# Kernel optimization log

Hardware: AMD Instinct MI355X
Metric: run time of the kernel (lower is better)

Reference implementation:

```python
import jax, jax.numpy as jnp
import numpy as np

B, N, E, P, PH, H = 4, 512, 768, 64, 32, 8
D = E // H  # 96
FFN = 3072

def _ln(x, g, b, eps=1e-5):
    mu = jnp.mean(x, axis=-1, keepdims=True)
    var = jnp.mean((x - mu) ** 2, axis=-1, keepdims=True)
    return (x - mu) * jax.lax.rsqrt(var + eps) * g + b

def setup_inputs() -> dict:
    key = jax.random.key(0)
    ks = iter(jax.random.split(key, 80))
    def f(*s):
        return jax.random.normal(next(ks), s, jnp.float32) * 0.02
    ones = lambda *s: jnp.ones(s, jnp.float32)
    zeros = lambda *s: jnp.zeros(s, jnp.float32)
    return {
        'x': jax.random.normal(next(ks), (B, N, E), jnp.float32),
        'pair': jax.random.normal(next(ks), (B, N, N, P), jnp.float32) * 0.5,
        'attn_mask': zeros(B, 1, N, N),
        'op_mask': ones(B, N, 1),
        'op_norm': ones(1) / N,
        'nlist': jax.random.randint(next(ks), (B, N, 64), 0, N),
        'wq': f(E, E), 'wk': f(E, E), 'wv': f(E, E),
        'wg': f(E, E), 'bg': zeros(E),
        'wo': f(E, E), 'bo': zeros(E),
        'ln_pair_g': ones(P), 'ln_pair_b': zeros(P),
        'wb': f(H, P), 'bb': zeros(H),
        'ln_attn_g': ones(E), 'ln_attn_b': zeros(E),
        'ln_ffn_g': ones(E), 'ln_ffn_b': zeros(E),
        'w_ffn1': f(FFN, E), 'b_ffn1': zeros(FFN),
        'w_ffn2': f(E, FFN), 'b_ffn2': zeros(E),
        'ln_opm_g': ones(E), 'ln_opm_b': zeros(E),
        'w_opm_in': f(2 * PH, E), 'b_opm_in': zeros(2 * PH),
        'w_opm_out': f(P, PH * PH), 'b_opm_out': zeros(P),
        'ln_tm_g': ones(P), 'ln_tm_b': zeros(P),
        'w_tm_abp': f(2 * PH, P), 'b_tm_abp': zeros(2 * PH),
        'w_tm_abg': f(2 * PH, P), 'b_tm_abg': zeros(2 * PH),
        'w_tm_g': f(P, P), 'b_tm_g': zeros(P),
        'w_tm_z': f(P, PH), 'b_tm_z': zeros(P),
        'ln_tmo_g': ones(PH), 'ln_tmo_b': zeros(PH),
        'ln_pffn_g': ones(P), 'ln_pffn_b': zeros(P),
        'w_pffn1': f(P, P), 'b_pffn1': zeros(P),
        'w_pffn2': f(P, P), 'b_pffn2': zeros(P),
    }

def _forward(x, pair, attn_mask, op_mask, op_norm, wq, wk, wv, wg, bg, wo, bo,
             ln_pair_g, ln_pair_b, wb, bb, ln_attn_g, ln_attn_b,
             ln_ffn_g, ln_ffn_b, w_ffn1, b_ffn1, w_ffn2, b_ffn2,
             ln_opm_g, ln_opm_b, w_opm_in, b_opm_in, w_opm_out, b_opm_out,
             ln_tm_g, ln_tm_b, w_tm_abp, b_tm_abp, w_tm_abg, b_tm_abg,
             w_tm_g, b_tm_g, w_tm_z, b_tm_z, ln_tmo_g, ln_tmo_b,
             ln_pffn_g, ln_pffn_b, w_pffn1, b_pffn1, w_pffn2, b_pffn2):
    Bx, Nx, _ = x.shape
    # --- gated pair-bias self-attention (pre-LN, eval mode: dropout = identity) ---
    h = _ln(x, ln_attn_g, ln_attn_b)
    pn = _ln(pair, ln_pair_g, ln_pair_b)               # AtomAttention pair LayerNorm
    bias = jnp.einsum('bijp,hp->bhij', pn, wb) + bb[None, :, None, None]
    q = (h @ wq.T).reshape(Bx, Nx, H, D).transpose(0, 2, 1, 3) * (D ** -0.5)
    k = (h @ wk.T).reshape(Bx, Nx, H, D).transpose(0, 2, 1, 3)
    v = (h @ wv.T).reshape(Bx, Nx, H, D).transpose(0, 2, 1, 3)
    attn = jax.nn.softmax(jnp.einsum('bhid,bhjd->bhij', q, k) + attn_mask + bias, axis=-1)
    o = jnp.einsum('bhij,bhjd->bhid', attn, v).transpose(0, 2, 1, 3).reshape(Bx, Nx, E)
    o = jax.nn.sigmoid(h @ wg.T + bg) * o              # sigmoid output gate
    x = x + (o @ wo.T + bo)
    # --- atom transition MLP ---
    h = _ln(x, ln_ffn_g, ln_ffn_b)
    x = x + (jax.nn.gelu(h @ w_ffn1.T + b_ffn1, approximate=False) @ w_ffn2.T + b_ffn2)
    # --- OuterProduct pair update (fused: avoids [B,N,N,PH*PH] intermediate) ---
    h = _ln(x, ln_opm_g, ln_opm_b)
    ab = (h @ w_opm_in.T + b_opm_in) * op_mask
    a_o, b_o = jnp.split(ab, 2, axis=-1)               # each [B,N,PH]
    z = jnp.einsum('bid,bje,pde->bijp', a_o, b_o, w_opm_out.reshape(P, PH, PH)) + b_opm_out
    pair = pair + z * op_norm
    # --- triangle multiplication ---
    zp = _ln(pair, ln_tm_g, ln_tm_b)
    gpr = zp @ w_tm_g.T + b_tm_g                       # gate (no sigmoid, matches source)
    ab = (zp @ w_tm_abp.T + b_tm_abp) * jax.nn.sigmoid(zp @ w_tm_abg.T + b_tm_abg)
    a_t, b_t = jnp.split(ab, 2, axis=-1)               # each [B,N,N,PH]
    t = jnp.einsum('bijh,bkjh->bhik', a_t, b_t) + jnp.einsum('bjih,bjkh->bhik', a_t, b_t)
    t = _ln(t.transpose(0, 2, 3, 1), ln_tmo_g, ln_tmo_b) @ w_tm_z.T + b_tm_z
    pair = pair + gpr * t
    # --- pair transition MLP ---
    zp = _ln(pair, ln_pffn_g, ln_pffn_b)
    pair = pair + (jax.nn.gelu(zp @ w_pffn1.T + b_pffn1, approximate=False) @ w_pffn2.T + b_pffn2)
    return x, pair

def reference(x, pair, attn_mask, op_mask, op_norm, nlist, wq, wk, wv, wg, bg, wo, bo,
              ln_pair_g, ln_pair_b, wb, bb, ln_attn_g, ln_attn_b,
              ln_ffn_g, ln_ffn_b, w_ffn1, b_ffn1, w_ffn2, b_ffn2,
              ln_opm_g, ln_opm_b, w_opm_in, b_opm_in, w_opm_out, b_opm_out,
              ln_tm_g, ln_tm_b, w_tm_abp, b_tm_abp, w_tm_abg, b_tm_abg,
              w_tm_g, b_tm_g, w_tm_z, b_tm_z, ln_tmo_g, ln_tmo_b,
              ln_pffn_g, ln_pffn_b, w_pffn1, b_pffn1, w_pffn2, b_pffn2):
    del nlist  # accepted by the torch module but unused in the math
    return _forward(x, pair, attn_mask, op_mask, op_norm, wq, wk, wv, wg, bg, wo, bo,
                    ln_pair_g, ln_pair_b, wb, bb, ln_attn_g, ln_attn_b,
                    ln_ffn_g, ln_ffn_b, w_ffn1, b_ffn1, w_ffn2, b_ffn2,
                    ln_opm_g, ln_opm_b, w_opm_in, b_opm_in, w_opm_out, b_opm_out,
                    ln_tm_g, ln_tm_b, w_tm_abp, b_tm_abp, w_tm_abg, b_tm_abg,
                    w_tm_g, b_tm_g, w_tm_z, b_tm_z, ln_tmo_g, ln_tmo_b,
                    ln_pffn_g, ln_pffn_b, w_pffn1, b_pffn1, w_pffn2, b_pffn2)
```

## Files before the change

kernel.cpp:

```cpp
#include <hip/hip_runtime.h>
#include <hip/hip_bf16.h>
#include <math.h>

#define Nn 512
#define Ee 768
#define Pp 64
#define PHh 32
#define Hh 8
#define Dd 96
#define NNe 262144
#define LNEPS 1e-5f

typedef __attribute__((ext_vector_type(8))) short bf8;
typedef __attribute__((ext_vector_type(4))) short bf4;
typedef __attribute__((ext_vector_type(4))) float f32x4;
#define MFMA(a,b,c) __builtin_amdgcn_mfma_f32_16x16x32_bf16(a,b,c,0,0,0)

__device__ __forceinline__ short f2bf(float f) {
  unsigned u = __builtin_bit_cast(unsigned, f);
  unsigned r = (u + 0x7fffu + ((u >> 16) & 1u)) >> 16;
  return (short)r;
}
__device__ __forceinline__ float bf2f(short s) {
  unsigned u = ((unsigned)(unsigned short)s) << 16;
// ... 117 lines not shown
      bf8 b0 = *(const bf8*)&Bs[(wc * 32 + llo) * 72 + ks * 32 + lhi * 8];
      bf8 b1 = *(const bf8*)&Bs[(wc * 32 + 16 + llo) * 72 + ks * 32 + lhi * 8];
      acc[0][0] = MFMA(a0, b0, acc[0][0]);
      acc[0][1] = MFMA(a0, b1, acc[0][1]);
      acc[1][0] = MFMA(a1, b0, acc[1][0]);
      acc[1][1] = MFMA(a1, b1, acc[1][1]);
    }
    __syncthreads();
  }
#pragma unroll
  for (int mi = 0; mi < 2; ++mi) {
    int gmb = m0 + wr * 32 + mi * 16 + lhi * 4;
#pragma unroll
    for (int ni = 0; ni < 2; ++ni) {
      int gn = n0 + wc * 32 + ni * 16 + llo;
      if (gn >= N) continue;
      float bv = bias ? bias[gn] : 0.f;
      float vr[4];
#pragma unroll
      for (int r = 0; r < 4; ++r) {
        float v = acc[mi][ni][r] + bv;
        if (resid) {
          float rv = resid[(long)(gmb + r) * ldr + gn];
          if (act == 2) v = sigmoidf_(rv) * acc[mi][ni][r];
          else v += rv;
        }
        if (act == 1) v = gelu_exact(v);
        vr[r] = v;
      }
      if (outF) {
#pragma unroll
        for (int r = 0; r < 4; ++r) outF[(long)(gmb + r) * ldf + gn] = vr[r];
      }
      if (outB) {
        if (vtrans) {
          bf4 pk;
#pragma unroll
          for (int r = 0; r < 4; ++r) pk[r] = f2bf(vr[r]);
          *(bf4*)(outB + ((long)((gmb >> 9) * 768 + gn) * 512 + (gmb & 511))) = pk;
        } else {
#pragma unroll
          for (int r = 0; r < 4; ++r) outB[(long)(gmb + r) * ldob + gn] = f2bf(vr[r]);
        }
      }
    }
  }
}

__global__ __launch_bounds__(256) void gemm_qkvg(
    const short* __restrict__ A, const short* __restrict__ W,
    short* __restrict__ q_bf, short* __restrict__ k_bf,
    short* __restrict__ vT_bf, float* __restrict__ gb,
    const float* __restrict__ bg) {
  __shared__ __align__(16) short As[64 * 72];
  __shared__ __align__(16) short Bs[64 * 72];
  int m0 = blockIdx.y * 64, n0 = blockIdx.x * 64;
  int sec = n0 / 768;
  int cbase = n0 - sec * 768;
  int tid = threadIdx.x;
  int wv = tid >> 6, lane = tid & 63;
  int wr = wv >> 1, wc = wv & 1;
  int lhi = lane >> 4, llo = lane & 15;
  int r4 = tid >> 2, c8 = (tid & 3) * 8;
  f32x4 acc[2][2] = {};
  for (int k0 = 0; k0 < 768; k0 += 64) {
    *(bf8*)&As[r4 * 72 + c8] = *(const bf8*)(A + (long)(m0 + r4) * 768 + k0 + c8);
    *(bf8*)&As[r4 * 72 + 32 + c8] =
        *(const bf8*)(A + (long)(m0 + r4) * 768 + k0 + 32 + c8);
    *(bf8*)&Bs[r4 * 72 + c8] = *(const bf8*)(W + (long)(n0 + r4) * 768 + k0 + c8);
    *(bf8*)&Bs[r4 * 72 + 32 + c8] =
        *(const bf8*)(W + (long)(n0 + r4) * 768 + k0 + 32 + c8);
    __syncthreads();
#pragma unroll
    for (int ks = 0; ks < 2; ++ks) {
      bf8 a0 = *(const bf8*)&As[(wr * 32 + llo) * 72 + ks * 32 + lhi * 8];
      bf8 a1 = *(const bf8*)&As[(wr * 32 + 16 + llo) * 72 + ks * 32 + lhi * 8];
      bf8 b0 = *(const bf8*)&Bs[(wc * 32 + llo) * 72 + ks * 32 + lhi * 8];
      bf8 b1 = *(const bf8*)&Bs[(wc * 32 + 16 + llo) * 72 + ks * 32 + lhi * 8];
      acc[0][0] = MFMA(a0, b0, acc[0][0]);
      acc[0][1] = MFMA(a0, b1, acc[0][1]);
      acc[1][0] = MFMA(a1, b0, acc[1][0]);
      acc[1][1] = MFMA(a1, b1, acc[1][1]);
    }
    __syncthreads();
  }
#pragma unroll
  for (int mi = 0; mi < 2; ++mi) {
    int gmb = m0 + wr * 32 + mi * 16 + lhi * 4;
#pragma unroll
    for (int ni = 0; ni < 2; ++ni) {
      int cn = cbase + wc * 32 + ni * 16 + llo;
      if (sec == 0) {
#pragma unroll
        for (int r = 0; r < 4; ++r) q_bf[(long)(gmb + r) * 768 + cn] = f2bf(acc[mi][ni][r]);
      } else if (sec == 1) {
#pragma unroll
        for (int r = 0; r < 4; ++r) k_bf[(long)(gmb + r) * 768 + cn] = f2bf(acc[mi][ni][r]);
      } else if (sec == 2) {
        bf4 pk;
#pragma unroll
        for (int r = 0; r < 4; ++r) pk[r] = f2bf(acc[mi][ni][r]);
        *(bf4*)(vT_bf + ((long)((gmb >> 9) * 768 + cn) * 512 + (gmb & 511))) = pk;
      } else {
        float bv = bg[cn];
#pragma unroll
        for (int r = 0; r < 4; ++r) gb[(long)(gmb + r) * 768 + cn] = acc[mi][ni][r] + bv;
      }
    }
  }
}

__global__ __launch_bounds__(256) void attn_fused(
    const short* __restrict__ q_bf, const short* __restrict__ k_bf,
    const short* __restrict__ bias_bf, const float* __restrict__ mask,
    short* __restrict__ out_bf) {
  int it = blockIdx.x, h = blockIdx.y, b = blockIdx.z;
  int tid = threadIdx.x;
  int wv = tid >> 6, lane = tid & 63;
  int lhi = lane >> 4, llo = lane & 15;
  int i0 = it * 16;
  long qoff = ((long)(b * 512 + i0)) * 768 + h * 96;
  bf8 qf[3];
#pragma unroll
  for (int ks = 0; ks < 3; ++ks)
    qf[ks] = *(const bf8*)(q_bf + qoff + (long)llo * 768 + ks * 32 + lhi * 8);
  long koff = ((long)b * 512) * 768 + h * 96;
  long bioff = (long)(b * 8 + h) * NNe + (long)i0 * 512;
  long moff = (long)b * NNe + (long)i0 * 512;
  float sv[8][4];
  int jb0 = wv * 128;
#pragma unroll
  for (int jf = 0; jf < 8; ++jf) {
    int jb = jb0 + jf * 16;
    f32x4 acc = {0.f, 0.f, 0.f, 0.f};
#pragma unroll
    for (int ks = 0; ks < 3; ++ks) {
      bf8 kf = *(const bf8*)(k_bf + koff + (long)(jb + llo) * 768 + ks * 32 + lhi * 8);
      acc = MFMA(qf[ks], kf, acc);
    }
#pragma unroll
    for (int r = 0; r < 4; ++r) {
      int irow = lhi * 4 + r;
      int j = jb + llo;
      float bia = bf2f(bias_bf[bioff + (long)irow * 512 + j]);
      float mk = mask[moff + (long)irow * 512 + j];
      sv[jf][r] = acc[r] + bia + mk;
    }
  }
  __shared__ float redA[4][20];
  __shared__ float redB[4][20];
  float rmax[4];
#pragma unroll
  for (int r = 0; r < 4; ++r) {
    float m = sv[0][r];
#pragma unroll
    for (int jf = 1; jf < 8; ++jf) m = fmaxf(m, sv[jf][r]);
#pragma unroll
    for (int off = 1; off < 16; off <<= 1) m = fmaxf(m, __shfl_xor(m, off, 16));
    if (llo == 0) redA[wv][lhi * 4 + r] = m;
  }
// ... 75 lines not shown
    int h = l >> 6, c = l & 63;
    Wb[h * 72 + c] = (h < 8) ? wb_a[h * 64 + c] : (short)0;
  }
  int e = tid & 63, q = tid >> 6;
  f32x4 v4[4];
  float s = 0.f, ss = 0.f;
#pragma unroll
  for (int k = 0; k < 4; ++k) {
    v4[k] = *(const f32x4*)(base + (long)e * 64 + q * 16 + k * 4);
#pragma unroll
    for (int u = 0; u < 4; ++u) { float v = v4[k][u]; s += v; ss += v * v; }
  }
  sp[q][0][e] = s; sp[q][1][e] = ss;
  __syncthreads();
  float ts = sp[0][0][e] + sp[1][0][e] + sp[2][0][e] + sp[3][0][e];
  float tss = sp[0][1][e] + sp[1][1][e] + sp[2][1][e] + sp[3][1][e];
  float mu = ts * 0.015625f, var = tss * 0.015625f - mu * mu;
  float rs = rsqrtf(var + LNEPS);
#pragma unroll
  for (int k = 0; k < 4; ++k) {
    bf4 pk;
#pragma unroll
    for (int u = 0; u < 4; ++u) {
      int c = q * 16 + k * 4 + u;
      pk[u] = f2bf((v4[k][u] - mu) * rs * gam[c] + bet[c]);
    }
    *(bf4*)&Zb[e * 72 + q * 16 + k * 4] = pk;
  }
  __syncthreads();
  int wv = tid >> 6, lane = tid & 63;
  int lhi = lane >> 4, llo = lane & 15;
  int n0 = wv * 16;
  f32x4 acc = {0.f, 0.f, 0.f, 0.f};
#pragma unroll
  for (int ks = 0; ks < 2; ++ks) {
    bf8 a = *(const bf8*)&Wb[llo * 72 + ks * 32 + lhi * 8];
    bf8 bz = *(const bf8*)&Zb[(n0 + llo) * 72 + ks * 32 + lhi * 8];
    acc = MFMA(a, bz, acc);
  }
  int elem = n0 + llo;
#pragma unroll
  for (int r = 0; r < 4; ++r) {
    int h = lhi * 4 + r;
    if (h < 8) bias[(long)(b * 8 + h) * NNe + ein + elem] = f2bf(acc[r] + bbv[h]);
  }
}

__global__ __launch_bounds__(256) void opm_ab_fused(
    const float* __restrict__ pair_in, const short* __restrict__ Tb,
    const short* __restrict__ bo_bf, const float* __restrict__ b_out,
    const float* __restrict__ op_norm, const float* __restrict__ gam,
    const float* __restrict__ bet, const short* __restrict__ wp_a,
    const float* __restrict__ b_abp, const short* __restrict__ wg_a,
    const float* __restrict__ b_abg, float* __restrict__ pair1,
    short* __restrict__ aN, short* __restrict__ bN) {
  int jt = blockIdx.x;
  int i = blockIdx.y;
  int tid = threadIdx.x;
  __shared__ __align__(16) short Tsb[64 * 40];
  __shared__ __align__(16) short Bob[64 * 40];
  __shared__ __align__(16) short Zb[64 * 72];
  __shared__ __align__(16) short Wp[64 * 72];
  __shared__ __align__(16) short Wg[64 * 72];
  __shared__ float spS[64][9];
  __shared__ float spQ[64][9];
  int wv = tid >> 6, lane = tid & 63;
  int wr = wv >> 1, wc = wv & 1;
  int lhi = lane >> 4, llo = lane & 15;
  int chb = wr * 32 + lhi * 4;
  {
    int p = tid >> 2, e8 = (tid & 3) * 8;
    *(bf8*)&Tsb[p * 40 + e8] = *(const bf8*)(Tb + (long)i * 2048 + p * 32 + e8);
    *(bf8*)&Bob[p * 40 + e8] = *(const bf8*)(bo_bf + (long)(jt * 64 + p) * 32 + e8);
  }
  for (int l = tid; l < 512; l += 256) {
    int r = l >> 3, c8 = (l & 7) * 8;
    *(bf8*)&Wp[r * 72 + c8] = *(const bf8*)(wp_a + r * 64 + c8);
    *(bf8*)&Wg[r * 72 + c8] = *(const bf8*)(wg_a + r * 64 + c8);
  }
  long ebase = (long)i * 512 + jt * 64;
  const float* pbase = pair_in + ebase * 64;
  f32x4 x[2][2];
#pragma unroll
  for (int mi = 0; mi < 2; ++mi)
#pragma unroll
    for (int ni = 0; ni < 2; ++ni)
      x[mi][ni] = *(const f32x4*)(pbase + (long)(wc * 32 + ni * 16 + llo) * 64 +
                                  chb + mi * 16);
  __syncthreads();
  f32x4 acc[2][2] = {};
  {
    bf8 a0 = *(const bf8*)&Tsb[(wr * 32 + llo) * 40 + lhi * 8];
    bf8 a1 = *(const bf8*)&Tsb[(wr * 32 + 16 + llo) * 40 + lhi * 8];
    bf8 b0 = *(const bf8*)&Bob[(wc * 32 + llo) * 40 + lhi * 8];
    bf8 b1 = *(const bf8*)&Bob[(wc * 32 + 16 + llo) * 40 + lhi * 8];
    acc[0][0] = MFMA(a0, b0, acc[0][0]);
    acc[0][1] = MFMA(a0, b1, acc[0][1]);
    acc[1][0] = MFMA(a1, b0, acc[1][0]);
    acc[1][1] = MFMA(a1, b1, acc[1][1]);
  }
  float nrm = op_norm[0];
#pragma unroll
  for (int mi = 0; mi < 2; ++mi) {
    f32x4 bo4 = *(const f32x4*)(b_out + chb + mi * 16);
#pragma unroll
    for (int ni = 0; ni < 2; ++ni)
#pragma unroll
      for (int r = 0; r < 4; ++r)
        x[mi][ni][r] += (acc[mi][ni][r] + bo4[r]) * nrm;
  }
#pragma unroll
  for (int mi = 0; mi < 2; ++mi)
#pragma unroll
    for (int ni = 0; ni < 2; ++ni)
      *(f32x4*)(pair1 + (ebase + wc * 32 + ni * 16 + llo) * 64 + chb + mi * 16) =
          x[mi][ni];
#pragma unroll
  for (int ni = 0; ni < 2; ++ni) {
    float s = 0.f, ss = 0.f;
#pragma unroll
    for (int mi = 0; mi < 2; ++mi)
#pragma unroll
      for (int r = 0; r < 4; ++r) { float v = x[mi][ni][r]; s += v; ss += v * v; }
    int e = wc * 32 + ni * 16 + llo;
    spS[e][wr * 4 + lhi] = s;
    spQ[e][wr * 4 + lhi] = ss;
  }
  __syncthreads();
  float mu1[2], rs1[2];
#pragma unroll
  for (int ni = 0; ni < 2; ++ni) {
    int e = wc * 32 + ni * 16 + llo;
    float s = 0.f, q2 = 0.f;
#pragma unroll
    for (int k = 0; k < 8; ++k) { s += spS[e][k]; q2 += spQ[e][k]; }
    float mu = s * 0.015625f, var = q2 * 0.015625f - mu * mu;
    mu1[ni] = mu; rs1[ni] = rsqrtf(var + LNEPS);
  }
#pragma unroll
  for (int mi = 0; mi < 2; ++mi) {
    f32x4 gv = *(const f32x4*)(gam + chb + mi * 16);
    f32x4 bv = *(const f32x4*)(bet + chb + mi * 16);
#pragma unroll
    for (int ni = 0; ni < 2; ++ni) {
      int e = wc * 32 + ni * 16 + llo;
      bf4 pk;
#pragma unroll
      for (int r = 0; r < 4; ++r)
        pk[r] = f2bf((x[mi][ni][r] - mu1[ni]) * rs1[ni] * gv[r] + bv[r]);
      *(bf4*)&Zb[e * 72 + chb + mi * 16] = pk;
    }
  }
  __syncthreads();
  f32x4 ap[2][2] = {};
  f32x4 ag[2][2] = {};
#pragma unroll
  for (int ks = 0; ks < 2; ++ks) {
    bf8 z0 = *(const bf8*)&Zb[(wr * 32 + llo) * 72 + ks * 32 + lhi * 8];
    bf8 z1 = *(const bf8*)&Zb[(wr * 32 + 16 + llo) * 72 + ks * 32 + lhi * 8];
    bf8 p0 = *(const bf8*)&Wp[(wc * 32 + llo) * 72 + ks * 32 + lhi * 8];
    bf8 p1 = *(const bf8*)&Wp[(wc * 32 + 16 + llo) * 72 + ks * 32 + lhi * 8];
    bf8 g0 = *(const bf8*)&Wg[(wc * 32 + llo) * 72 + ks * 32 + lhi * 8];
    bf8 g1 = *(const bf8*)&Wg[(wc * 32 + 16 + llo) * 72 + ks * 32 + lhi * 8];
    ap[0][0] = MFMA(z0, p0, ap[0][0]);
    ap[0][1] = MFMA(z0, p1, ap[0][1]);
    ap[1][0] = MFMA(z1, p0, ap[1][0]);
    ap[1][1] = MFMA(z1, p1, ap[1][1]);
    ag[0][0] = MFMA(z0, g0, ag[0][0]);
    ag[0][1] = MFMA(z0, g1, ag[0][1]);
    ag[1][0] = MFMA(z1, g0, ag[1][0]);
    ag[1][1] = MFMA(z1, g1, ag[1][1]);
  }
#pragma unroll
  for (int mi = 0; mi < 2; ++mi) {
    int elemb = wr * 32 + mi * 16 + lhi * 4;
#pragma unroll
    for (int ni = 0; ni < 2; ++ni) {
      int ch = wc * 32 + ni * 16 + llo;
      float bp = b_abp[ch], bg = b_abg[ch];
      bf4 pack;
#pragma unroll
      for (int r = 0; r < 4; ++r)
        pack[r] = f2bf((ap[mi][ni][r] + bp) * sigmoidf_(ag[mi][ni][r] + bg));
      short* dst = (ch < 32) ? (aN + (long)ch * NNe) : (bN + (long)(ch - 32) * NNe);
      *(bf4*)(dst + ebase + elemb) = pack;
    }
  }
}

__global__ __launch_bounds__(512) void tm_tri_mfma(const short* __restrict__ aN,
                                                   const short* __restrict__ bN,
                                                   short* __restrict__ t_out) {
  int h = blockIdx.z;
  int i0 = blockIdx.y * 128, k0 = blockIdx.x * 128;
  const short* A = aN + (long)h * NNe;
  const short* B = bN + (long)h * NNe;
  __shared__ __align__(16) short A1[128 * 40];
  __shared__ __align__(16) short B1[128 * 40];
  __shared__ __align__(16) short A2[128 * 40];
  __shared__ __align__(16) short B2[128 * 40];
  int tid = threadIdx.x;
  int wv = tid >> 6, lane = tid & 63;
  int wr = wv >> 2, wc = wv & 3;
  int lhi = lane >> 4, llo = lane & 15;
  int r1 = tid >> 2, cp = (tid & 3) * 8;
  int s2 = tid >> 5, cg = (tid & 31) * 4;
  f32x4 acc[4][2] = {};
  for (int j0 = 0; j0 < 512; j0 += 32) {
    *(bf8*)&A1[r1 * 40 + cp] = *(const bf8*)(A + (long)(i0 + r1) * 512 + j0 + cp);
    *(bf8*)&B1[r1 * 40 + cp] = *(const bf8*)(B + (long)(k0 + r1) * 512 + j0 + cp);
    bf4 va0 = *(const bf4*)(A + (long)(j0 + 2 * s2) * 512 + i0 + cg);
    bf4 va1 = *(const bf4*)(A + (long)(j0 + 2 * s2 + 1) * 512 + i0 + cg);
    bf4 vb0 = *(const bf4*)(B + (long)(j0 + 2 * s2) * 512 + k0 + cg);
    bf4 vb1 = *(const bf4*)(B + (long)(j0 + 2 * s2 + 1) * 512 + k0 + cg);
#pragma unroll
    for (int q = 0; q < 4; ++q) {
      unsigned pa = (unsigned)(unsigned short)va0[q] |
                    ((unsigned)(unsigned short)va1[q] << 16);
      unsigned pb = (unsigned)(unsigned short)vb0[q] |
                    ((unsigned)(unsigned short)vb1[q] << 16);
      *(unsigned*)&A2[(cg + q) * 40 + 2 * s2] = pa;
      *(unsigned*)&B2[(cg + q) * 40 + 2 * s2] = pb;
    }
    __syncthreads();
    bf8 bfr[2], dfr[2];
#pragma unroll
    for (int ni = 0; ni < 2; ++ni) {
      bfr[ni] = *(const bf8*)&B1[(wc * 32 + ni * 16 + llo) * 40 + lhi * 8];
      dfr[ni] = *(const bf8*)&B2[(wc * 32 + ni * 16 + llo) * 40 + lhi * 8];
    }
#pragma unroll
    for (int mi = 0; mi < 4; ++mi) {
      bf8 a = *(const bf8*)&A1[(wr * 64 + mi * 16 + llo) * 40 + lhi * 8];
      acc[mi][0] = MFMA(a, bfr[0], acc[mi][0]);
      acc[mi][1] = MFMA(a, bfr[1], acc[mi][1]);
    }
#pragma unroll
    for (int mi = 0; mi < 4; ++mi) {
      bf8 c = *(const bf8*)&A2[(wr * 64 + mi * 16 + llo) * 40 + lhi * 8];
      acc[mi][0] = MFMA(c, dfr[0], acc[mi][0]);
      acc[mi][1] = MFMA(c, dfr[1], acc[mi][1]);
    }
    __syncthreads();
  }
  short* tp = t_out + (long)h * NNe;
#pragma unroll
  for (int mi = 0; mi < 4; ++mi)
#pragma unroll
    for (int ni = 0; ni < 2; ++ni) {
      int row = i0 + wr * 64 + mi * 16 + lhi * 4;
      int col = k0 + wc * 32 + ni * 16 + llo;
#pragma unroll
      for (int r = 0; r < 4; ++r) tp[(long)(row + r) * 512 + col] = f2bf(acc[mi][ni][r]);
    }
}

__global__ __launch_bounds__(256) void upd_pffn_fused(
    float* __restrict__ pb, const short* __restrict__ t_in,
    const float* __restrict__ g_tm, const float* __restrict__ b_tm,
    const short* __restrict__ wg_a, const float* __restrict__ b_g,
    const short* __restrict__ wz_a, const float* __restrict__ b_z,
    const float* __restrict__ g_tmo, const float* __restrict__ b_tmo,
    const float* __restrict__ g_pf, const float* __restrict__ b_pf,
    const short* __restrict__ w1_a, const float* __restrict__ b1,
    const short* __restrict__ w2_a, const float* __restrict__ b2) {
  __shared__ __align__(16) short Zb[64 * 72];
  __shared__ __align__(16) short Tlb[64 * 40];
  __shared__ __align__(16) short Wbuf[64 * 72];
  __shared__ __align__(16) short Wzb[64 * 40];
  __shared__ float spS[64][9];
  __shared__ float spQ[64][9];
  __shared__ float spB[4][2][72];
  int tid = threadIdx.x;
  long e0 = (long)blockIdx.x * 64;
  float* base = pb + e0 * 64;
  int wv = tid >> 6, lane = tid & 63;
  int wr = wv >> 1, wc = wv & 1;
  int lhi = lane >> 4, llo = lane & 15;
  int chb = wr * 32 + lhi * 4;
  int r0 = tid >> 3, c0 = (tid & 7) * 8;
  int r1 = (tid + 256) >> 3, c1 = ((tid + 256) & 7) * 8;
  bf8 w1r0, w1r1, w2r0, w2r1;
  {
    *(bf8*)&Wbuf[r0 * 72 + c0] = *(const bf8*)(wg_a + r0 * 64 + c0);
    *(bf8*)&Wbuf[r1 * 72 + c1] = *(const bf8*)(wg_a + r1 * 64 + c1);
    w1r0 = *(const bf8*)(w1_a + r0 * 64 + c0);
    w1r1 = *(const bf8*)(w1_a + r1 * 64 + c1);
    w2r0 = *(const bf8*)(w2_a + r0 * 64 + c0);
    w2r1 = *(const bf8*)(w2_a + r1 * 64 + c1);
    int rz = tid >> 2, cz = (tid & 3) * 8;
    *(bf8*)&Wzb[rz * 40 + cz] = *(const bf8*)(wz_a + rz * 32 + cz);
  }
  f32x4 x[2][2];
#pragma unroll
  for (int mi = 0; mi < 2; ++mi)
#pragma unroll
    for (int ni = 0; ni < 2; ++ni)
      x[mi][ni] = *(const f32x4*)(base + (long)(wc * 32 + ni * 16 + llo) * 64 +
                                  chb + mi * 16);
#pragma unroll
  for (int ni = 0; ni < 2; ++ni) {
    float s = 0.f, ss = 0.f;
#pragma unroll
    for (int mi = 0; mi < 2; ++mi)
#pragma unroll
      for (int r = 0; r < 4; ++r) { float v = x[mi][ni][r]; s += v; ss += v * v; }
    int e = wc * 32 + ni * 16 + llo;
    spS[e][wr * 4 + lhi] = s;
    spQ[e][wr * 4 + lhi] = ss;
  }
  int te = tid & 63, tq = tid >> 6;
  float tt[8];
  {
    float sB = 0.f, ssB = 0.f;
#pragma unroll
    for (int k = 0; k < 8; ++k) {
      float v = bf2f(t_in[(long)(tq * 8 + k) * NNe + e0 + te]);
      tt[k] = v; sB += v; ssB += v * v;
    }
    spB[tq][0][te] = sB; spB[tq][1][te] = ssB;
  }
  __syncthreads();
  {
    float ts = spB[0][0][te] + spB[1][0][te] + spB[2][0][te] + spB[3][0][te];
    float tss = spB[0][1][te] + spB[1][1][te] + spB[2][1][te] + spB[3][1][te];
    float mu = ts * 0.03125f, var = tss * 0.03125f - mu * mu;
    float rs = rsqrtf(var + LNEPS);
    bf8 pk;
#pragma unroll
    for (int k = 0; k < 8; ++k) {
      int c = tq * 8 + k;
      pk[k] = f2bf((tt[k] - mu) * rs * g_tmo[c] + b_tmo[c]);
    }
    *(bf8*)&Tlb[te * 40 + tq * 8] = pk;
  }
  float mu1[2], rs1[2];
#pragma unroll
  for (int ni = 0; ni < 2; ++ni) {
    int e = wc * 32 + ni * 16 + llo;
    float s = 0.f, q2 = 0.f;
#pragma unroll
    for (int k = 0; k < 8; ++k) { s += spS[e][k]; q2 += spQ[e][k]; }
    float mu = s * 0.015625f, var = q2 * 0.015625f - mu * mu;
    mu1[ni] = mu; rs1[ni] = rsqrtf(var + LNEPS);
  }
#pragma unroll
  for (int mi = 0; mi < 2; ++mi) {
    f32x4 gv = *(const f32x4*)(g_tm + chb + mi * 16);
    f32x4 bv = *(const f32x4*)(b_tm + chb + mi * 16);
#pragma unroll
    for (int ni = 0; ni < 2; ++ni) {
      int e = wc * 32 + ni * 16 + llo;
      bf4 pk;
#pragma unroll
      for (int r = 0; r < 4; ++r)
        pk[r] = f2bf((x[mi][ni][r] - mu1[ni]) * rs1[ni] * gv[r] + bv[r]);
      *(bf4*)&Zb[e * 72 + chb + mi * 16] = pk;
    }
  }
  __syncthreads();
  f32x4 accg[2][2] = {};
  f32x4 accz[2][2] = {};
#pragma unroll
  for (int ks = 0; ks < 2; ++ks) {
    bf8 a0 = *(const bf8*)&Wbuf[(wr * 32 + llo) * 72 + ks * 32 + lhi * 8];
    bf8 a1 = *(const bf8*)&Wbuf[(wr * 32 + 16 + llo) * 72 + ks * 32 + lhi * 8];
    bf8 z0 = *(const bf8*)&Zb[(wc * 32 + llo) * 72 + ks * 32 + lhi * 8];
    bf8 z1 = *(const bf8*)&Zb[(wc * 32 + 16 + llo) * 72 + ks * 32 + lhi * 8];
    accg[0][0] = MFMA(a0, z0, accg[0][0]);
    accg[0][1] = MFMA(a0, z1, accg[0][1]);
    accg[1][0] = MFMA(a1, z0, accg[1][0]);
    accg[1][1] = MFMA(a1, z1, accg[1][1]);
  }
  {
    bf8 a0 = *(const bf8*)&Wzb[(wr * 32 + llo) * 40 + lhi * 8];
    bf8 a1 = *(const bf8*)&Wzb[(wr * 32 + 16 + llo) * 40 + lhi * 8];
    bf8 t0 = *(const bf8*)&Tlb[(wc * 32 + llo) * 40 + lhi * 8];
    bf8 t1 = *(const bf8*)&Tlb[(wc * 32 + 16 + llo) * 40 + lhi * 8];
    accz[0][0] = MFMA(a0, t0, accz[0][0]);
    accz[0][1] = MFMA(a0, t1, accz[0][1]);
    accz[1][0] = MFMA(a1, t0, accz[1][0]);
    accz[1][1] = MFMA(a1, t1, accz[1][1]);
  }
#pragma unroll
  for (int mi = 0; mi < 2; ++mi) {
    f32x4 bgv = *(const f32x4*)(b_g + chb + mi * 16);
    f32x4 bzv = *(const f32x4*)(b_z + chb + mi * 16);
#pragma unroll
// ... 37 lines not shown
      for (int r = 0; r < 4; ++r)
        pk[r] = f2bf((x[mi][ni][r] - mu1[ni]) * rs1[ni] * gv[r] + bv[r]);
      *(bf4*)&Zb[e * 72 + chb + mi * 16] = pk;
    }
  }
  __syncthreads();
  f32x4 acc1[2][2] = {};
#pragma unroll
  for (int ks = 0; ks < 2; ++ks) {
    bf8 a0 = *(const bf8*)&Wbuf[(wr * 32 + llo) * 72 + ks * 32 + lhi * 8];
    bf8 a1 = *(const bf8*)&Wbuf[(wr * 32 + 16 + llo) * 72 + ks * 32 + lhi * 8];
    bf8 z0 = *(const bf8*)&Zb[(wc * 32 + llo) * 72 + ks * 32 + lhi * 8];
    bf8 z1 = *(const bf8*)&Zb[(wc * 32 + 16 + llo) * 72 + ks * 32 + lhi * 8];
    acc1[0][0] = MFMA(a0, z0, acc1[0][0]);
    acc1[0][1] = MFMA(a0, z1, acc1[0][1]);
    acc1[1][0] = MFMA(a1, z0, acc1[1][0]);
    acc1[1][1] = MFMA(a1, z1, acc1[1][1]);
  }
  __syncthreads();
  *(bf8*)&Wbuf[r0 * 72 + c0] = w2r0;
  *(bf8*)&Wbuf[r1 * 72 + c1] = w2r1;
#pragma unroll
  for (int mi = 0; mi < 2; ++mi) {
    f32x4 bv = *(const f32x4*)(b1 + chb + mi * 16);
#pragma unroll
    for (int ni = 0; ni < 2; ++ni) {
      int e = wc * 32 + ni * 16 + llo;
      bf4 pk;
#pragma unroll
      for (int r = 0; r < 4; ++r) pk[r] = f2bf(gelu_exact(acc1[mi][ni][r] + bv[r]));
      *(bf4*)&Zb[e * 72 + chb + mi * 16] = pk;
    }
  }
  __syncthreads();
  f32x4 acc2[2][2] = {};
#pragma unroll
  for (int ks = 0; ks < 2; ++ks) {
    bf8 a0 = *(const bf8*)&Wbuf[(wr * 32 + llo) * 72 + ks * 32 + lhi * 8];
    bf8 a1 = *(const bf8*)&Wbuf[(wr * 32 + 16 + llo) * 72 + ks * 32 + lhi * 8];
    bf8 z0 = *(const bf8*)&Zb[(wc * 32 + llo) * 72 + ks * 32 + lhi * 8];
    bf8 z1 = *(const bf8*)&Zb[(wc * 32 + 16 + llo) * 72 + ks * 32 + lhi * 8];
    acc2[0][0] = MFMA(a0, z0, acc2[0][0]);
    acc2[0][1] = MFMA(a0, z1, acc2[0][1]);
    acc2[1][0] = MFMA(a1, z0, acc2[1][0]);
    acc2[1][1] = MFMA(a1, z1, acc2[1][1]);
  }
#pragma unroll
  for (int mi = 0; mi < 2; ++mi) {
    f32x4 bv = *(const f32x4*)(b2 + chb + mi * 16);
#pragma unroll
    for (int ni = 0; ni < 2; ++ni) {
#pragma unroll
      for (int r = 0; r < 4; ++r) x[mi][ni][r] += acc2[mi][ni][r] + bv[r];
      *(f32x4*)(base + (long)(wc * 32 + ni * 16 + llo) * 64 + chb + mi * 16) =
          x[mi][ni];
    }
  }
}

extern "C" void kernel_launch(void* const* d_in, const int* in_sizes, int n_in,
                              void* d_out, int out_size, void* d_ws, size_t ws_size,
                              hipStream_t stream) {
  const float* x = (const float*)d_in[0];
  const float* pair = (const float*)d_in[1];
  const float* attn_mask = (const float*)d_in[2];
  const float* op_mask = (const float*)d_in[3];
  const float* op_norm = (const float*)d_in[4];
  const float* wq = (const float*)d_in[6];
  const float* wk = (const float*)d_in[7];
  const float* wv_ = (const float*)d_in[8];
  const float* wg = (const float*)d_in[9];
  const float* bg = (const float*)d_in[10];
  const float* wo = (const float*)d_in[11];
  const float* bo = (const float*)d_in[12];
  const float* ln_pair_g = (const float*)d_in[13];
  const float* ln_pair_b = (const float*)d_in[14];
  const float* wb = (const float*)d_in[15];
  const float* bb = (const float*)d_in[16];
  const float* ln_attn_g = (const float*)d_in[17];
  const float* ln_attn_b = (const float*)d_in[18];
  const float* ln_ffn_g = (const float*)d_in[19];
  const float* ln_ffn_b = (const float*)d_in[20];
  const float* w_ffn1 = (const float*)d_in[21];
  const float* b_ffn1 = (const float*)d_in[22];
  const float* w_ffn2 = (const float*)d_in[23];
  const float* b_ffn2 = (const float*)d_in[24];
  const float* ln_opm_g = (const float*)d_in[25];
  const float* ln_opm_b = (const float*)d_in[26];
  const float* w_opm_in = (const float*)d_in[27];
  const float* b_opm_in = (const float*)d_in[28];
  const float* w_opm_out = (const float*)d_in[29];
  const float* b_opm_out = (const float*)d_in[30];
  const float* ln_tm_g = (const float*)d_in[31];
  const float* ln_tm_b = (const float*)d_in[32];
  const float* w_tm_abp = (const float*)d_in[33];
  const float* b_tm_abp = (const float*)d_in[34];
  const float* w_tm_abg = (const float*)d_in[35];
  const float* b_tm_abg = (const float*)d_in[36];
  const float* w_tm_g = (const float*)d_in[37];
  const float* b_tm_g = (const float*)d_in[38];
  const float* w_tm_z = (const float*)d_in[39];
  const float* b_tm_z = (const float*)d_in[40];
  const float* ln_tmo_g = (const float*)d_in[41];
  const float* ln_tmo_b = (const float*)d_in[42];
  const float* ln_pffn_g = (const float*)d_in[43];
  const float* ln_pffn_b = (const float*)d_in[44];
  const float* w_pffn1 = (const float*)d_in[45];
  const float* b_pffn1 = (const float*)d_in[46];
  const float* w_pffn2 = (const float*)d_in[47];
  const float* b_pffn2 = (const float*)d_in[48];

  float* ws = (float*)d_ws;
  short* wbf = (short*)ws;
  short* wq_bf = wbf + 0;
  short* wo_bf = wbf + 2359296;
  short* wf1_bf = wbf + 2949120;
  short* wf2_bf = wbf + 5308416;
  short* wop_bf = wbf + 7667712;
  short* wb_a = wbf + 7716864;
  short* wabp_a = wbf + 7717376;
  short* wabg_a = wbf + 7721472;
  short* wtg_a = wbf + 7725568;
  short* wtz_a = wbf + 7729664;
  short* wp1_a = wbf + 7731712;
  short* wp2_a = wbf + 7735808;

  short* h_bf = (short*)(ws + 3869952);
  short* q_bf = (short*)(ws + 4656384);
  short* k_bf = (short*)(ws + 5442816);
  short* vT_bf = (short*)(ws + 6229248);
  float* gb = ws + 7015680;
  short* gb_bf = (short*)(ws + 10161408);
  float* x1b = ws + 10947840;
  short* biasb_bf = (short*)(ws + 12520704);
  short* attn_bf = (short*)(ws + 16715008);
  short* mffn_bf = (short*)(ws + 20909312);
  float* abb = ws + 24055040;
  short* abb_bf = (short*)(ws + 24186112);
  short* Tb_bf = (short*)(ws + 24218880);
  short* aNb = (short*)(ws + 4656384);
  short* bNb = (short*)(ws + 8850688);
  short* t_bf = (short*)(ws + 13044992);

  float* xo = (float*)d_out;
  float* pair1 = xo + 1572864;

  const float qscale = 0.1020620726159658f;

  castw_kernel<<<30144, 256, 0, stream>>>(wq, wk, wv_, wg, wo, w_ffn1, w_ffn2, w_opm_in,
                                          wbf, qscale);
  castw2_kernel<<<90, 256, 0, stream>>>(wb, w_tm_abp, w_tm_abg, w_tm_g, w_tm_z,
                                        w_pffn1, w_pffn2, wb_a);
  ln_bf_kernel<<<2048, 256, 0, stream>>>(x, h_bf, ln_attn_g, ln_attn_b, 768);
  gemm_qkvg<<<dim3(48, 32, 1), 256, 0, stream>>>(h_bf, wq_bf, q_bf, k_bf, vT_bf, gb, bg);
  pair_bias_mfma<<<16384, 256, 0, stream>>>(pair, ln_pair_g, ln_pair_b, wb_a, bb, biasb_bf);
  attn_fused<<<dim3(32, 8, 4), 256, 0, stream>>>(q_bf, k_bf, biasb_bf, attn_mask, attn_bf);
  gemm_bf<<<dim3(2, 8, 32), 256, 0, stream>>>(attn_bf, 512, 2097152, 262144,
                                              vT_bf, 512, 393216, 49152,
                                              nullptr, 0, 393216, 96, gb_bf, 768,
                                              gb, 768, 393216, 96, nullptr,
                                              512, 96, 512, 2, 0, 8);
  gemm_bf<<<dim3(12, 32, 1), 256, 0, stream>>>(gb_bf, 768, 0, 0, wo_bf, 768, 0, 0,
                                               x1b, 768, 0, 0, nullptr, 0,
                                               x, 768, 0, 0, bo,
                                               2048, 768, 768, 0, 0, 1);
  ln_bf_kernel<<<2048, 256, 0, stream>>>(x1b, h_bf, ln_ffn_g, ln_ffn_b, 768);
  gemm_bf<<<dim3(48, 32, 1), 256, 0, stream>>>(h_bf, 768, 0, 0, wf1_bf, 768, 0, 0,
                                               nullptr, 0, 0, 0, mffn_bf, 3072,
                                               nullptr, 0, 0, 0, b_ffn1,
                                               2048, 3072, 768, 1, 0, 1);
  gemm_bf<<<dim3(12, 32, 1), 256, 0, stream>>>(mffn_bf, 3072, 0, 0, wf2_bf, 3072, 0, 0,
                                               xo, 768, 0, 0, nullptr, 0,
                                               x1b, 768, 0, 0, b_ffn2,
                                               2048, 768, 3072, 0, 0, 1);
  ln_bf_kernel<<<2048, 256, 0, stream>>>(xo, h_bf, ln_opm_g, ln_opm_b, 768);
  gemm_bf<<<dim3(1, 32, 1), 256, 0, stream>>>(h_bf, 768, 0, 0, wop_bf, 768, 0, 0,
                                              abb, 64, 0, 0, nullptr, 0,
                                              nullptr, 0, 0, 0, b_opm_in,
                                              2048, 64, 768, 0, 0, 1);
  opmask_kernel<<<512, 256, 0, stream>>>(abb, op_mask, abb_bf);
  opm_T_kernel<<<dim3(256, 64, 1), dim3(32, 8, 1), 0, stream>>>(abb, w_opm_out, Tb_bf);
  for (int b = 0; b < 4; ++b) {
    const float* pin = pair + (long)b * NNe * 64;
    float* pbb = pair1 + (long)b * NNe * 64;
    opm_ab_fused<<<dim3(8, 512, 1), 256, 0, stream>>>(
        pin, Tb_bf + (long)b * 1048576, abb_bf + (long)b * 16384, b_opm_out, op_norm,
        ln_tm_g, ln_tm_b, wabp_a, b_tm_abp, wabg_a, b_tm_abg, pbb, aNb, bNb);
    tm_tri_mfma<<<dim3(4, 4, 32), 512, 0, stream>>>(aNb, bNb, t_bf);
    upd_pffn_fused<<<4096, 256, 0, stream>>>(
        pbb, t_bf, ln_tm_g, ln_tm_b, wtg_a, b_tm_g, wtz_a, b_tm_z,
        ln_tmo_g, ln_tmo_b, ln_pffn_g, ln_pffn_b, wp1_a, b_pffn1, wp2_a, b_pffn2);
  }
}
```

Before: 949.8 us.

## Enlarge QKVG/FFN1 GEMM tiles, recompute OPM update instead of storing pair1, remap tri blocks

The QKVG GEMM and a new dedicated FFN1 GEMM move to 128x128 tiles with a 4x4 MFMA accumulator per wave and a K step of 32. This raises operand reuse per LDS load and cuts the block count. opm_ab_fused no longer writes the intermediate pair1 tensor. Instead upd_pffn_fused reads the original pair input and recomputes the small outer-product-mean MFMA and bias, which avoids a full fp32 pair write and read per batch at the cost of redundant compute. tm_tri_mfma also remaps its block index so that consecutive blocks are interleaved across heads, likely to spread memory traffic differently.

```diff
diff --git a/kernel.cpp b/kernel.cpp
--- a/kernel.cpp
+++ b/kernel.cpp
@@ -193,9 +193,9 @@
     short* __restrict__ q_bf, short* __restrict__ k_bf,
     short* __restrict__ vT_bf, float* __restrict__ gb,
     const float* __restrict__ bg) {
-  __shared__ __align__(16) short As[64 * 72];
-  __shared__ __align__(16) short Bs[64 * 72];
-  int m0 = blockIdx.y * 64, n0 = blockIdx.x * 64;
+  __shared__ __align__(16) short As[128 * 40];
+  __shared__ __align__(16) short Bs[128 * 40];
+  int m0 = blockIdx.y * 128, n0 = blockIdx.x * 128;
   int sec = n0 / 768;
   int cbase = n0 - sec * 768;
   int tid = threadIdx.x;
@@ -203,34 +203,35 @@
   int wr = wv >> 1, wc = wv & 1;
   int lhi = lane >> 4, llo = lane & 15;
   int r4 = tid >> 2, c8 = (tid & 3) * 8;
-  f32x4 acc[2][2] = {};
-  for (int k0 = 0; k0 < 768; k0 += 64) {
-    *(bf8*)&As[r4 * 72 + c8] = *(const bf8*)(A + (long)(m0 + r4) * 768 + k0 + c8);
-    *(bf8*)&As[r4 * 72 + 32 + c8] =
-        *(const bf8*)(A + (long)(m0 + r4) * 768 + k0 + 32 + c8);
-    *(bf8*)&Bs[r4 * 72 + c8] = *(const bf8*)(W + (long)(n0 + r4) * 768 + k0 + c8);
-    *(bf8*)&Bs[r4 * 72 + 32 + c8] =
-        *(const bf8*)(W + (long)(n0 + r4) * 768 + k0 + 32 + c8);
+  f32x4 acc[4][4] = {};
+  for (int k0 = 0; k0 < 768; k0 += 32) {
+    *(bf8*)&As[r4 * 40 + c8] = *(const bf8*)(A + (long)(m0 + r4) * 768 + k0 + c8);
+    *(bf8*)&As[(r4 + 64) * 40 + c8] =
+        *(const bf8*)(A + (long)(m0 + r4 + 64) * 768 + k0 + c8);
+    *(bf8*)&Bs[r4 * 40 + c8] = *(const bf8*)(W + (long)(n0 + r4) * 768 + k0 + c8);
+    *(bf8*)&Bs[(r4 + 64) * 40 + c8] =
+        *(const bf8*)(W + (long)(n0 + r4 + 64) * 768 + k0 + c8);
     __syncthreads();
-#pragma unroll
-    for (int ks = 0; ks < 2; ++ks) {
-      bf8 a0 = *(const bf8*)&As[(wr * 32 + llo) * 72 + ks * 32 + lhi * 8];
-      bf8 a1 = *(const bf8*)&As[(wr * 32 + 16 + llo) * 72 + ks * 32 + lhi * 8];
-      bf8 b0 = *(const bf8*)&Bs[(wc * 32 + llo) * 72 + ks * 32 + lhi * 8];
-      bf8 b1 = *(const bf8*)&Bs[(wc * 32 + 16 + llo) * 72 + ks * 32 + lhi * 8];
-      acc[0][0] = MFMA(a0, b0, acc[0][0]);
-      acc[0][1] = MFMA(a0, b1, acc[0][1]);
-      acc[1][0] = MFMA(a1, b0, acc[1][0]);
-      acc[1][1] = MFMA(a1, b1, acc[1][1]);
-    }
+    bf8 af[4], bfm[4];
+#pragma unroll
+    for (int mi = 0; mi < 4; ++mi)
+      af[mi] = *(const bf8*)&As[(wr * 64 + mi * 16 + llo) * 40 + lhi * 8];
+#pragma unroll
+    for (int ni = 0; ni < 4; ++ni)
+      bfm[ni] = *(const bf8*)&Bs[(wc * 64 + ni * 16 + llo) * 40 + lhi * 8];
+#pragma unroll
+    for (int mi = 0; mi < 4; ++mi)
+#pragma unroll
+      for (int ni = 0; ni < 4; ++ni)
+        acc[mi][ni] = MFMA(af[mi], bfm[ni], acc[mi][ni]);
     __syncthreads();
   }
 #pragma unroll
-  for (int mi = 0; mi < 2; ++mi) {
-    int gmb = m0 + wr * 32 + mi * 16 + lhi * 4;
-#pragma unroll
-    for (int ni = 0; ni < 2; ++ni) {
-      int cn = cbase + wc * 32 + ni * 16 + llo;
+  for (int mi = 0; mi < 4; ++mi) {
+    int gmb = m0 + wr * 64 + mi * 16 + lhi * 4;
+#pragma unroll
+    for (int ni = 0; ni < 4; ++ni) {
+      int cn = cbase + wc * 64 + ni * 16 + llo;
       if (sec == 0) {
 #pragma unroll
         for (int r = 0; r < 4; ++r) q_bf[(long)(gmb + r) * 768 + cn] = f2bf(acc[mi][ni][r]);
@@ -247,6 +248,54 @@
 #pragma unroll
         for (int r = 0; r < 4; ++r) gb[(long)(gmb + r) * 768 + cn] = acc[mi][ni][r] + bv;
       }
+    }
+  }
+}
+
+__global__ __launch_bounds__(256) void gemm_ffn1(
+    const short* __restrict__ A, const short* __restrict__ W,
+    short* __restrict__ outB, const float* __restrict__ bias) {
+  __shared__ __align__(16) short As[128 * 40];
+  __shared__ __align__(16) short Bs[128 * 40];
+  int m0 = blockIdx.y * 128, n0 = blockIdx.x * 128;
+  int tid = threadIdx.x;
+  int wv = tid >> 6, lane = tid & 63;
+  int wr = wv >> 1, wc = wv & 1;
+  int lhi = lane >> 4, llo = lane & 15;
+  int r4 = tid >> 2, c8 = (tid & 3) * 8;
+  f32x4 acc[4][4] = {};
+  for (int k0 = 0; k0 < 768; k0 += 32) {
+    *(bf8*)&As[r4 * 40 + c8] = *(const bf8*)(A + (long)(m0 + r4) * 768 + k0 + c8);
+    *(bf8*)&As[(r4 + 64) * 40 + c8] =
+        *(const bf8*)(A + (long)(m0 + r4 + 64) * 768 + k0 + c8);
+    *(bf8*)&Bs[r4 * 40 + c8] = *(const bf8*)(W + (long)(n0 + r4) * 768 + k0 + c8);
+    *(bf8*)&Bs[(r4 + 64) * 40 + c8] =
+        *(const bf8*)(W + (long)(n0 + r4 + 64) * 768 + k0 + c8);
+    __syncthreads();
+    bf8 af[4], bfm[4];
+#pragma unroll
+    for (int mi = 0; mi < 4; ++mi)
+      af[mi] = *(const bf8*)&As[(wr * 64 + mi * 16 + llo) * 40 + lhi * 8];
+#pragma unroll
+    for (int ni = 0; ni < 4; ++ni)
+      bfm[ni] = *(const bf8*)&Bs[(wc * 64 + ni * 16 + llo) * 40 + lhi * 8];
+#pragma unroll
+    for (int mi = 0; mi < 4; ++mi)
+#pragma unroll
+      for (int ni = 0; ni < 4; ++ni)
+        acc[mi][ni] = MFMA(af[mi], bfm[ni], acc[mi][ni]);
+    __syncthreads();
+  }
+#pragma unroll
+  for (int mi = 0; mi < 4; ++mi) {
+    int gmb = m0 + wr * 64 + mi * 16 + lhi * 4;
+#pragma unroll
+    for (int ni = 0; ni < 4; ++ni) {
+      int gn = n0 + wc * 64 + ni * 16 + llo;
+      float bv = bias[gn];
+#pragma unroll
+      for (int r = 0; r < 4; ++r)
+        outB[(long)(gmb + r) * 3072 + gn] = f2bf(gelu_exact(acc[mi][ni][r] + bv));
     }
   }
 }
@@ -428,7 +477,7 @@
     const float* __restrict__ op_norm, const float* __restrict__ gam,
     const float* __restrict__ bet, const short* __restrict__ wp_a,
     const float* __restrict__ b_abp, const short* __restrict__ wg_a,
-    const float* __restrict__ b_abg, float* __restrict__ pair1,
+    const float* __restrict__ b_abg,
     short* __restrict__ aN, short* __restrict__ bN) {
   int jt = blockIdx.x;
   int i = blockIdx.y;
@@ -486,12 +535,6 @@
         x[mi][ni][r] += (acc[mi][ni][r] + bo4[r]) * nrm;
   }
 #pragma unroll
-  for (int mi = 0; mi < 2; ++mi)
-#pragma unroll
-    for (int ni = 0; ni < 2; ++ni)
-      *(f32x4*)(pair1 + (ebase + wc * 32 + ni * 16 + llo) * 64 + chb + mi * 16) =
-          x[mi][ni];
-#pragma unroll
   for (int ni = 0; ni < 2; ++ni) {
     float s = 0.f, ss = 0.f;
 #pragma unroll
@@ -567,8 +610,11 @@
 __global__ __launch_bounds__(512) void tm_tri_mfma(const short* __restrict__ aN,
                                                    const short* __restrict__ bN,
                                                    short* __restrict__ t_out) {
-  int h = blockIdx.z;
-  int i0 = blockIdx.y * 128, k0 = blockIdx.x * 128;
+  int lin = blockIdx.z * 16 + blockIdx.y * 4 + blockIdx.x;
+  int vid = (lin & 7) * 64 + (lin >> 3);
+  int h = vid >> 4;
+  int rem = vid & 15;
+  int i0 = (rem >> 2) * 128, k0 = (rem & 3) * 128;
   const short* A = aN + (long)h * NNe;
   const short* B = bN + (long)h * NNe;
   __shared__ __align__(16) short A1[128 * 40];
@@ -632,7 +678,10 @@
 }
 
 __global__ __launch_bounds__(256) void upd_pffn_fused(
-    float* __restrict__ pb, const short* __restrict__ t_in,
+    const float* __restrict__ pin, float* __restrict__ pout,
+    const short* __restrict__ t_in,
+    const short* __restrict__ Tb, const short* __restrict__ bo_bf,
+    const float* __restrict__ b_out, const float* __restrict__ op_norm,
     const float* __restrict__ g_tm, const float* __restrict__ b_tm,
     const short* __restrict__ wg_a, const float* __restrict__ b_g,
     const short* __restrict__ wz_a, const float* __restrict__ b_z,
@@ -644,12 +693,15 @@
   __shared__ __align__(16) short Tlb[64 * 40];
   __shared__ __align__(16) short Wbuf[64 * 72];
   __shared__ __align__(16) short Wzb[64 * 40];
+  __shared__ __align__(16) short Tsb[64 * 40];
+  __shared__ __align__(16) short Bob[64 * 40];
   __shared__ float spS[64][9];
   __shared__ float spQ[64][9];
   __shared__ float spB[4][2][72];
   int tid = threadIdx.x;
   long e0 = (long)blockIdx.x * 64;
-  float* base = pb + e0 * 64;
+  int i = (int)(e0 >> 9);
+  int jt = (int)((e0 >> 6) & 7);
   int wv = tid >> 6, lane = tid & 63;
   int wr = wv >> 1, wc = wv & 1;
   int lhi = lane >> 4, llo = lane & 15;
@@ -666,25 +718,17 @@
     w2r1 = *(const bf8*)(w2_a + r1 * 64 + c1);
     int rz = tid >> 2, cz = (tid & 3) * 8;
     *(bf8*)&Wzb[rz * 40 + cz] = *(const bf8*)(wz_a + rz * 32 + cz);
+    int p = tid >> 2, e8 = (tid & 3) * 8;
+    *(bf8*)&Tsb[p * 40 + e8] = *(const bf8*)(Tb + (long)i * 2048 + p * 32 + e8);
+    *(bf8*)&Bob[p * 40 + e8] = *(const bf8*)(bo_bf + (long)(jt * 64 + p) * 32 + e8);
   }
   f32x4 x[2][2];
 #pragma unroll
   for (int mi = 0; mi < 2; ++mi)
 #pragma unroll
     for (int ni = 0; ni < 2; ++ni)
-      x[mi][ni] = *(const f32x4*)(base + (long)(wc * 32 + ni * 16 + llo) * 64 +
+      x[mi][ni] = *(const f32x4*)(pin + (e0 + wc * 32 + ni * 16 + llo) * 64 +
                                   chb + mi * 16);
-#pragma unroll
-  for (int ni = 0; ni < 2; ++ni) {
-    float s = 0.f, ss = 0.f;
-#pragma unroll
-    for (int mi = 0; mi < 2; ++mi)
-#pragma unroll
-      for (int r = 0; r < 4; ++r) { float v = x[mi][ni][r]; s += v; ss += v * v; }
-    int e = wc * 32 + ni * 16 + llo;
-    spS[e][wr * 4 + lhi] = s;
-    spQ[e][wr * 4 + lhi] = ss;
-  }
   int te = tid & 63, tq = tid >> 6;
   float tt[8];
   {
@@ -710,6 +754,39 @@
     }
     *(bf8*)&Tlb[te * 40 + tq * 8] = pk;
   }
+  {
+    f32x4 acc[2][2] = {};
+    bf8 a0 = *(const bf8*)&Tsb[(wr * 32 + llo) * 40 + lhi * 8];
+    bf8 a1 = *(const bf8*)&Tsb[(wr * 32 + 16 + llo) * 40 + lhi * 8];
+    bf8 b0 = *(const bf8*)&Bob[(wc * 32 + llo) * 40 + lhi * 8];
+    bf8 b1 = *(const bf8*)&Bob[(wc * 32 + 16 + llo) * 40 + lhi * 8];
+    acc[0][0] = MFMA(a0, b0, acc[0][0]);
+    acc[0][1] = MFMA(a0, b1, acc[0][1]);
+    acc[1][0] = MFMA(a1, b0, acc[1][0]);
+    acc[1][1] = MFMA(a1, b1, acc[1][1]);
+    float nrm = op_norm[0];
+#pragma unroll
+    for (int mi = 0; mi < 2; ++mi) {
+      f32x4 bo4 = *(const f32x4*)(b_out + chb + mi * 16);
+#pragma unroll
+      for (int ni = 0; ni < 2; ++ni)
+#pragma unroll
+        for (int r = 0; r < 4; ++r)
+          x[mi][ni][r] += (acc[mi][ni][r] + bo4[r]) * nrm;
+    }
+  }
+#pragma unroll
+  for (int ni = 0; ni < 2; ++ni) {
+    float s = 0.f, ss = 0.f;
+#pragma unroll
+    for (int mi = 0; mi < 2; ++mi)
+#pragma unroll
+      for (int r = 0; r < 4; ++r) { float v = x[mi][ni][r]; s += v; ss += v * v; }
+    int e = wc * 32 + ni * 16 + llo;
+    spS[e][wr * 4 + lhi] = s;
+    spQ[e][wr * 4 + lhi] = ss;
+  }
+  __syncthreads();
   float mu1[2], rs1[2];
 #pragma unroll
   for (int ni = 0; ni < 2; ++ni) {
@@ -853,7 +930,7 @@
     for (int ni = 0; ni < 2; ++ni) {
 #pragma unroll
       for (int r = 0; r < 4; ++r) x[mi][ni][r] += acc2[mi][ni][r] + bv[r];
-      *(f32x4*)(base + (long)(wc * 32 + ni * 16 + llo) * 64 + chb + mi * 16) =
+      *(f32x4*)(pout + (e0 + wc * 32 + ni * 16 + llo) * 64 + chb + mi * 16) =
           x[mi][ni];
     }
   }
@@ -953,7 +1030,7 @@
   castw2_kernel<<<90, 256, 0, stream>>>(wb, w_tm_abp, w_tm_abg, w_tm_g, w_tm_z,
                                         w_pffn1, w_pffn2, wb_a);
   ln_bf_kernel<<<2048, 256, 0, stream>>>(x, h_bf, ln_attn_g, ln_attn_b, 768);
-  gemm_qkvg<<<dim3(48, 32, 1), 256, 0, stream>>>(h_bf, wq_bf, q_bf, k_bf, vT_bf, gb, bg);
+  gemm_qkvg<<<dim3(24, 16, 1), 256, 0, stream>>>(h_bf, wq_bf, q_bf, k_bf, vT_bf, gb, bg);
   pair_bias_mfma<<<16384, 256, 0, stream>>>(pair, ln_pair_g, ln_pair_b, wb_a, bb, biasb_bf);
   attn_fused<<<dim3(32, 8, 4), 256, 0, stream>>>(q_bf, k_bf, biasb_bf, attn_mask, attn_bf);
   gemm_bf<<<dim3(2, 8, 32), 256, 0, stream>>>(attn_bf, 512, 2097152, 262144,
@@ -966,10 +1043,7 @@
                                                x, 768, 0, 0, bo,
                                                2048, 768, 768, 0, 0, 1);
   ln_bf_kernel<<<2048, 256, 0, stream>>>(x1b, h_bf, ln_ffn_g, ln_ffn_b, 768);
-  gemm_bf<<<dim3(48, 32, 1), 256, 0, stream>>>(h_bf, 768, 0, 0, wf1_bf, 768, 0, 0,
-                                               nullptr, 0, 0, 0, mffn_bf, 3072,
-                                               nullptr, 0, 0, 0, b_ffn1,
-                                               2048, 3072, 768, 1, 0, 1);
+  gemm_ffn1<<<dim3(24, 16, 1), 256, 0, stream>>>(h_bf, wf1_bf, mffn_bf, b_ffn1);
   gemm_bf<<<dim3(12, 32, 1), 256, 0, stream>>>(mffn_bf, 3072, 0, 0, wf2_bf, 3072, 0, 0,
                                                xo, 768, 0, 0, nullptr, 0,
                                                x1b, 768, 0, 0, b_ffn2,
@@ -986,10 +1060,12 @@
     float* pbb = pair1 + (long)b * NNe * 64;
     opm_ab_fused<<<dim3(8, 512, 1), 256, 0, stream>>>(
         pin, Tb_bf + (long)b * 1048576, abb_bf + (long)b * 16384, b_opm_out, op_norm,
-        ln_tm_g, ln_tm_b, wabp_a, b_tm_abp, wabg_a, b_tm_abg, pbb, aNb, bNb);
+        ln_tm_g, ln_tm_b, wabp_a, b_tm_abp, wabg_a, b_tm_abg, aNb, bNb);
     tm_tri_mfma<<<dim3(4, 4, 32), 512, 0, stream>>>(aNb, bNb, t_bf);
     upd_pffn_fused<<<4096, 256, 0, stream>>>(
-        pbb, t_bf, ln_tm_g, ln_tm_b, wtg_a, b_tm_g, wtz_a, b_tm_z,
+        pin, pbb, t_bf, Tb_bf + (long)b * 1048576, abb_bf + (long)b * 16384,
+        b_opm_out, op_norm,
+        ln_tm_g, ln_tm_b, wtg_a, b_tm_g, wtz_a, b_tm_z,
         ln_tmo_g, ln_tmo_b, ln_pffn_g, ln_pffn_b, wp1_a, b_pffn1, wp2_a, b_pffn2);
   }
 }
```

After: 907.0 us. 1.05x faster.
